# Kernel optimization log

Measured on AMD Instinct MI355X. Metric: run time of the kernel, lower is better.

The kernel has to match this reference:

```python
import jax, jax.numpy as jnp
import numpy as np

N = 100000
E = 1600000
IN_C, HID_C, OUT_C = 40, 64, 3


def _sage_params(key, f_in, f_out):
    k1, k2, k3 = jax.random.split(key, 3)
    s = 1.0 / np.sqrt(f_in)
    return (jax.random.uniform(k1, (f_in, f_out), jnp.float32, -s, s),  # W_neigh (lin_l)
            jax.random.uniform(k2, (f_in, f_out), jnp.float32, -s, s),  # W_root  (lin_r)
            jax.random.uniform(k3, (f_out,), jnp.float32, -s, s))       # bias


def setup_inputs() -> dict:
    key = jax.random.key(0)
    ks = jax.random.split(key, 8)
    x = jax.random.normal(ks[0], (N, IN_C), jnp.float32)
    edge_index = jax.random.randint(ks[1], (2, E), 0, N, jnp.int64)
    dims = [(IN_C, HID_C), (HID_C, HID_C), (HID_C, OUT_C),   # encoder
            (OUT_C, HID_C), (HID_C, HID_C), (HID_C, IN_C)]   # decoder
    names = ['enc1', 'enc2', 'enc3', 'dec1', 'dec2', 'dec3']
    out = {'x': x, 'edge_index': edge_index}
    for name, (fi, fo), k in zip(names, dims, ks[2:]):
        Wl, Wr, b = _sage_params(k, fi, fo)
        out[name + '_Wl'] = Wl
        out[name + '_Wr'] = Wr
        out[name + '_b'] = b
    return out


def _sage_conv(h, src, dst, inv_deg, Wl, Wr, b):
    # mean-aggregate neighbor features (messages src -> dst), then linear.
    msg_sum = jax.ops.segment_sum(h[src], dst, num_segments=N)  # [N, F_in]
    agg = msg_sum * inv_deg                                      # mean aggregation
    return agg @ Wl + h @ Wr + b


def reference(x, edge_index,
              enc1_Wl, enc1_Wr, enc1_b, enc2_Wl, enc2_Wr, enc2_b,
              enc3_Wl, enc3_Wr, enc3_b, dec1_Wl, dec1_Wr, dec1_b,
              dec2_Wl, dec2_Wr, dec2_b, dec3_Wl, dec3_Wr, dec3_b):
    src, dst = edge_index[0], edge_index[1]
    deg = jax.ops.segment_sum(jnp.ones((E,), jnp.float32), dst, num_segments=N)
    inv_deg = (1.0 / jnp.maximum(deg, 1.0))[:, None]
    # encoder
    h = jax.nn.relu(_sage_conv(x, src, dst, inv_deg, enc1_Wl, enc1_Wr, enc1_b))
    h = jax.nn.relu(_sage_conv(h, src, dst, inv_deg, enc2_Wl, enc2_Wr, enc2_b))
    z = _sage_conv(h, src, dst, inv_deg, enc3_Wl, enc3_Wr, enc3_b)
    # decoder
    h = jax.nn.relu(_sage_conv(z, src, dst, inv_deg, dec1_Wl, dec1_Wr, dec1_b))
    h = jax.nn.relu(_sage_conv(h, src, dst, inv_deg, dec2_Wl, dec2_Wr, dec2_b))
    x_rec = _sage_conv(h, src, dst, inv_deg, dec3_Wl, dec3_Wr, dec3_b)
    return (x_rec, z)
```

## Files before the change

### kernel.cpp

```cpp
#include <hip/hip_runtime.h>
#include <stdint.h>

#define NNODES 100000
#define NEDGES 1600000
#define NB 98
#define WIN 25000
#define NSL 32
#define SLICE 50000

typedef unsigned short ushort_t;
typedef __attribute__((ext_vector_type(8))) short bf16x8;
typedef __attribute__((ext_vector_type(4))) float f32x4;

__device__ __forceinline__ float b2f(ushort_t u) {
  union { float f; uint32_t i; } v; v.i = ((uint32_t)u) << 16; return v.f;
}
__device__ __forceinline__ float blo(uint32_t p) {
  union { float f; uint32_t i; } v; v.i = p << 16; return v.f;
}
__device__ __forceinline__ float bhi(uint32_t p) {
  union { float f; uint32_t i; } v; v.i = p & 0xffff0000u; return v.f;
}
__device__ __forceinline__ ushort_t f2b(float f) {
  union { float f; uint32_t i; } v; v.f = f;
  uint32_t r = (v.i + 0x7fffu + ((v.i >> 16) & 1u)) >> 16;
  return (ushort_t)r;
}
__device__ __forceinline__ uint32_t pack2(float lo, float hi) {
  return (uint32_t)f2b(lo) | ((uint32_t)f2b(hi) << 16);
}
__device__ __forceinline__ int clampn(int i) {
  return i < 0 ? 0 : (i >= NNODES ? NNODES - 1 : i);
}

__global__ void detect_k(const uint32_t* __restrict__ x, const uint32_t* __restrict__ ei,
                         int* __restrict__ flags) {
  if (blockIdx.x == 0 && threadIdx.x == 0) {
    int cf = 0, ci = 0;
    for (int i = 0; i < 256; ++i) {
      uint32_t u = x[i];
      uint32_t e = (u >> 7) & 0xFFu;
      if (e >= 100u && e <= 141u) cf++;
      if (ei[2 * i + 1] == 0u) ci++;
    }
    flags[0] = (cf >= 128) ? 1 : 0;
    flags[1] = (ci >= 128) ? 1 : 0;
  }
}

__global__ void zero_i32(int* __restrict__ p, int n) {
  int i = blockIdx.x * blockDim.x + threadIdx.x;
  if (i < n) p[i] = 0;
}

__global__ __launch_bounds__(256) void histw_k(const uint32_t* __restrict__ ei,
                                               int* __restrict__ degp,
                                               const int* __restrict__ flags) {
  __shared__ int h[WIN];
  int b = blockIdx.x;
  int w = b >> 5, s = b & 31;
  for (int j = threadIdx.x; j < WIN; j += 256) h[j] = 0;
  __syncthreads();
  int i64 = flags[1];
  int base = w * WIN;
  int e0 = s * SLICE, e1 = e0 + SLICE;
  for (int e = e0 + threadIdx.x; e < e1; e += 256) {
    int d = i64 ? (int)ei[2 * (size_t)NEDGES + 2 * (size_t)e] : (int)ei[(size_t)NEDGES + e];
    d = clampn(d);
    int j = d - base;
    if ((unsigned)j < (unsigned)WIN) atomicAdd(&h[j], 1);
  }
  __syncthreads();
  int* dp = degp + (size_t)s * NNODES + base;
  for (int j = threadIdx.x; j < WIN; j += 256) dp[j] = h[j];
}

__global__ void hreduce_k(int* __restrict__ degp, int* __restrict__ deg) {
  int n = blockIdx.x * blockDim.x + threadIdx.x;
  if (n >= NNODES) return;
  int run = 0;
  #pragma unroll
  for (int s = 0; s < NSL; ++s) {
    size_t idx = (size_t)s * NNODES + n;
    int t = degp[idx];
    degp[idx] = run;
    run += t;
  }
  deg[n] = run;
}

__global__ __launch_bounds__(1024) void scan1_k(const int* __restrict__ deg, int* __restrict__ bsum) {
  __shared__ int wsum[16];
  int tid = threadIdx.x;
  int i = blockIdx.x * 1024 + tid;
  int v = (i < NNODES) ? deg[i] : 0;
  #pragma unroll
  for (int d = 32; d >= 1; d >>= 1) v += __shfl_down(v, d);
  if ((tid & 63) == 0) wsum[tid >> 6] = v;
  __syncthreads();
  if (tid == 0) {
    int t = 0;
    #pragma unroll
    for (int w = 0; w < 16; ++w) t += wsum[w];
    bsum[blockIdx.x] = t;
  }
}

__global__ void scan2_k(int* __restrict__ bsum, int* __restrict__ offs) {
  if (blockIdx.x == 0 && threadIdx.x == 0) {
    int run = 0;
    for (int b = 0; b < NB; ++b) { int t = bsum[b]; bsum[b] = run; run += t; }
    offs[NNODES] = run;
  }
}

__global__ __launch_bounds__(1024) void scan3_k(const int* __restrict__ deg, const int* __restrict__ bsum,
                                                int* __restrict__ offs, int* __restrict__ cursor,
                                                float* __restrict__ invd) {
  __shared__ int wsum[16];
  int tid = threadIdx.x;
  int lane = tid & 63, wid = tid >> 6;
  int i = blockIdx.x * 1024 + tid;
  int v = (i < NNODES) ? deg[i] : 0;
  int s = v;
  #pragma unroll
  for (int d = 1; d < 64; d <<= 1) {
    int t = __shfl_up(s, d);
    if (lane >= d) s += t;
  }
  if (lane == 63) wsum[wid] = s;
  __syncthreads();
  int wprefix = 0;
  #pragma unroll
  for (int w = 0; w < 16; ++w)
    if (w < wid) wprefix += wsum[w];
  if (i < NNODES) {
    int excl = bsum[blockIdx.x] + wprefix + s - v;
    offs[i] = excl;
    cursor[i] = excl;
    invd[i] = 1.0f / fmaxf((float)v, 1.0f);
  }
}

__global__ __launch_bounds__(256) void scatters_k(const uint32_t* __restrict__ ei,
                                                  const int* __restrict__ offs,
                                                  const int* __restrict__ degp,
                                                  int* __restrict__ csr,
                                                  const int* __restrict__ flags) {
  __shared__ int cur[WIN];
  int b = blockIdx.x;
  int w = b >> 5, s = b & 31;
  int base = w * WIN;
  const int* dp = degp + (size_t)s * NNODES + base;
  for (int j = threadIdx.x; j < WIN; j += 256) cur[j] = offs[base + j] + dp[j];
  __syncthreads();
  int i64 = flags[1];
  int e0 = s * SLICE, e1 = e0 + SLICE;
  for (int e = e0 + threadIdx.x; e < e1; e += 256) {
    int d = i64 ? (int)ei[2 * (size_t)NEDGES + 2 * (size_t)e] : (int)ei[(size_t)NEDGES + e];
    d = clampn(d);
    int j = d - base;
    if ((unsigned)j < (unsigned)WIN) {
      int src = i64 ? (int)ei[2 * (size_t)e] : (int)ei[e];
      int p = atomicAdd(&cur[j], 1);
      if (p >= 0 && p < NEDGES) csr[p] = clampn(src);
    }
  }
}

template <bool BF16>
__global__ void cvt_packx_k(const void* __restrict__ src, uint32_t* __restrict__ dst, int npairs,
                            const int* __restrict__ flags) {
  if (flags[0] != (BF16 ? 1 : 0)) return;
  int i = blockIdx.x * blockDim.x + threadIdx.x;
  if (i < npairs) {
    if constexpr (BF16) dst[i] = ((const uint32_t*)src)[i];
    else {
      const float* s = (const float*)src;
      dst[i] = pack2(s[2 * i], s[2 * i + 1]);
    }
  }
}

template <bool BF16>
__global__ void cvt_outp_k(const uint32_t* __restrict__ src, void* __restrict__ dst, int npairs,
                           const int* __restrict__ flags) {
  if (flags[0] != (BF16 ? 1 : 0)) return;
  int i = blockIdx.x * blockDim.x + threadIdx.x;
  if (i < npairs) {
    if constexpr (BF16) ((uint32_t*)dst)[i] = src[i];
    else {
      uint32_t w = src[i];
      float* d = (float*)dst;
      d[2 * i] = blo(w);
      d[2 * i + 1] = bhi(w);
    }
  }
}

template <bool BF16>
__global__ void cvt_out_k(const float* __restrict__ src, void* __restrict__ dst, int n,
                          const int* __restrict__ flags) {
  if (flags[0] != (BF16 ? 1 : 0)) return;
  int i = blockIdx.x * blockDim.x + threadIdx.x;
  if (i < n) {
    if constexpr (BF16) ((ushort_t*)dst)[i] = f2b(src[i]);
    else ((float*)dst)[i] = src[i];
  }
}

struct WPtrs { const void* p[18]; int sz[18]; int off[18]; };

template <bool BF16>
__global__ void cvt_w_k(WPtrs w, float* __restrict__ dst, const int* __restrict__ flags) {
  if (flags[0] != (BF16 ? 1 : 0)) return;
  int a = blockIdx.x;
  int sz = w.sz[a], off = w.off[a];
  for (int t = threadIdx.x; t < sz; t += blockDim.x) {
    dst[off + t] = BF16 ? b2f(((const ushort_t*)w.p[a])[t]) : ((const float*)w.p[a])[t];
  }
}

template <bool ADD_U>
__global__ __launch_bounds__(256) void agg3_k(const float* __restrict__ feat, const int* __restrict__ csr,
                                              const int* __restrict__ offs, const float* __restrict__ invd,
                                              const float* __restrict__ u, float* __restrict__ out) {
  int n = blockIdx.x * blockDim.x + threadIdx.x;
  if (n >= NNODES) return;
  int k0 = offs[n], k1 = offs[n + 1];
  float a0 = 0.f, a1 = 0.f, a2 = 0.f;
  int k = k0;
  for (; k + 4 <= k1; k += 4) {
    const float* r0 = feat + (size_t)clampn(csr[k]) * 3;
    const float* r1 = feat + (size_t)clampn(csr[k + 1]) * 3;
    const float* r2 = feat + (size_t)clampn(csr[k + 2]) * 3;
    const float* r3 = feat + (size_t)clampn(csr[k + 3]) * 3;
    a0 += r0[0] + r1[0] + r2[0] + r3[0];
    a1 += r0[1] + r1[1] + r2[1] + r3[1];
    a2 += r0[2] + r1[2] + r2[2] + r3[2];
  }
  for (; k < k1; ++k) {
    const float* r = feat + (size_t)clampn(csr[k]) * 3;
    a0 += r[0]; a1 += r[1]; a2 += r[2];
  }
  float iv = invd[n];
  a0 *= iv; a1 *= iv; a2 *= iv;
  if constexpr (ADD_U) {
    a0 += u[(size_t)n * 3];
    a1 += u[(size_t)n * 3 + 1];
    a2 += u[(size_t)n * 3 + 2];
  }
  out[(size_t)n * 3]     = a0;
  out[(size_t)n * 3 + 1] = a1;
  out[(size_t)n * 3 + 2] = a2;
}

template <int PAIRS, bool ADD_U>
__global__ __launch_bounds__(256) void aggp2_k(const uint32_t* __restrict__ feat, const int* __restrict__ csr,
                                               const int* __restrict__ offs, const float* __restrict__ invd,
                                               const uint32_t* __restrict__ u, uint32_t* __restrict__ out) {
  int lane = threadIdx.x & 63;
  int n = (blockIdx.x * blockDim.x + threadIdx.x) >> 6;
  if (n >= NNODES) return;
  int half = lane >> 5;
  int p = lane & 31;
  int k0 = offs[n], k1 = offs[n + 1];
  float aL = 0.f, aH = 0.f;
  int k = k0;
  for (; k + 8 <= k1; k += 8) {
    int i0 = clampn(csr[k + half]), i1 = clampn(csr[k + 2 + half]);
    int i2 = clampn(csr[k + 4 + half]), i3 = clampn(csr[k + 6 + half]);
    if (p < PAIRS) {
      uint32_t w0 = feat[(size_t)i0 * PAIRS + p];
      uint32_t w1 = feat[(size_t)i1 * PAIRS + p];
      uint32_t w2 = feat[(size_t)i2 * PAIRS + p];
      uint32_t w3 = feat[(size_t)i3 * PAIRS + p];
      aL += blo(w0) + blo(w1) + blo(w2) + blo(w3);
      aH += bhi(w0) + bhi(w1) + bhi(w2) + bhi(w3);
    }
  }
  for (; k < k1; k += 2) {
    int kk = k + half;
    if (kk < k1 && p < PAIRS) {
      uint32_t w = feat[(size_t)clampn(csr[kk]) * PAIRS + p];
      aL += blo(w);
      aH += bhi(w);
    }
  }
  aL += __shfl_xor(aL, 32);
  aH += __shfl_xor(aH, 32);
  if (half == 0 && p < PAIRS) {
    float iv = invd[n];
    float vL = aL * iv, vH = aH * iv;
    if constexpr (ADD_U) {
      uint32_t uw = u[(size_t)n * PAIRS + p];
      vL += blo(uw);
      vH += bhi(uw);
    }
    out[(size_t)n * PAIRS + p] = pack2(vL, vH);
  }
}

template <int F_IN, int F_OUT, bool DUAL, bool RELU, bool PIN, bool POUT>
__global__ __launch_bounds__(256) void mgemm_k(const void* __restrict__ Av, const void* __restrict__ Bv,
                                               const float* __restrict__ W1, const float* __restrict__ W2,
                                               const float* __restrict__ Wb,
                                               void* __restrict__ C1v, void* __restrict__ C2v) {
  constexpr int KS = (F_IN + 31) / 32;
  constexpr int JT = (F_OUT + 15) / 16;
  constexpr int PP = F_IN / 2;
  int lane = threadIdx.x & 63;
  int wid  = threadIdx.x >> 6;
  int tile = blockIdx.x * 4 + wid;
  if (tile * 16 >= NNODES) return;
  int l15 = lane & 15, l4 = lane >> 4;

  bf16x8 w1f[KS][JT], w2f[KS][JT];
  float bv[JT];
  #pragma unroll
  for (int ks = 0; ks < KS; ++ks) {
    #pragma unroll
    for (int jt = 0; jt < JT; ++jt) {
      int col = jt * 16 + l15;
      #pragma unroll
      for (int j = 0; j < 8; ++j) {
        int k = ks * 32 + l4 * 8 + j;
        bool ok = (k < F_IN) && (col < F_OUT);
        w1f[ks][jt][j] = ok ? (short)f2b(W1[k * F_OUT + col]) : (short)0;
        w2f[ks][jt][j] = ok ? (short)f2b(W2[k * F_OUT + col]) : (short)0;
      }
    }
  }
  #pragma unroll
  for (int jt = 0; jt < JT; ++jt) {
    int col = jt * 16 + l15;
    bv[jt] = (col < F_OUT) ? Wb[col] : 0.f;
  }

  int row = tile * 16 + l15;
  bf16x8 af[KS], bfr[KS];
  if constexpr (PIN) {
    const uint32_t* Arow = (const uint32_t*)Av + (size_t)row * PP;
    #pragma unroll
    for (int ks = 0; ks < KS; ++ks) {
      #pragma unroll
      for (int w4 = 0; w4 < 4; ++w4) {
        int word = ks * 16 + l4 * 4 + w4;
        uint32_t v = (word < PP) ? Arow[word] : 0u;
        af[ks][2 * w4]     = (short)(v & 0xffffu);
        af[ks][2 * w4 + 1] = (short)(v >> 16);
      }
    }
    if constexpr (!DUAL) {
      const uint32_t* Brow = (const uint32_t*)Bv + (size_t)row * PP;
      #pragma unroll
      for (int ks = 0; ks < KS; ++ks) {
        #pragma unroll
        for (int w4 = 0; w4 < 4; ++w4) {
          int word = ks * 16 + l4 * 4 + w4;
          uint32_t v = (word < PP) ? Brow[word] : 0u;
          bfr[ks][2 * w4]     = (short)(v & 0xffffu);
          bfr[ks][2 * w4 + 1] = (short)(v >> 16);
        }
      }
    }
  } else {
    const float* Arow = (const float*)Av + (size_t)row * F_IN;
    #pragma unroll
    for (int ks = 0; ks < KS; ++ks) {
      #pragma unroll
      for (int j = 0; j < 8; ++j) {
        int k = ks * 32 + l4 * 8 + j;
        af[ks][j] = (k < F_IN) ? (short)f2b(Arow[k]) : (short)0;
      }
    }
    if constexpr (!DUAL) {
      const float* Brow = (const float*)Bv + (size_t)row * F_IN;
      #pragma unroll
      for (int ks = 0; ks < KS; ++ks) {
        #pragma unroll
        for (int j = 0; j < 8; ++j) {
          int k = ks * 32 + l4 * 8 + j;
          bfr[ks][j] = (k < F_IN) ? (short)f2b(Brow[k]) : (short)0;
        }
      }
    }
  }

  f32x4 acc1[JT], acc2[DUAL ? JT : 1];
  #pragma unroll
  for (int jt = 0; jt < JT; ++jt) {
    acc1[jt] = (f32x4)(0.f);
    if constexpr (DUAL) acc2[jt] = (f32x4)(0.f);
  }

  #pragma unroll
  for (int ks = 0; ks < KS; ++ks) {
    #pragma unroll
    for (int jt = 0; jt < JT; ++jt) {
      acc1[jt] = __builtin_amdgcn_mfma_f32_16x16x32_bf16(af[ks], w1f[ks][jt], acc1[jt], 0, 0, 0);
      if constexpr (DUAL)
        acc2[jt] = __builtin_amdgcn_mfma_f32_16x16x32_bf16(af[ks], w2f[ks][jt], acc2[jt], 0, 0, 0);
      else
        acc1[jt] = __builtin_amdgcn_mfma_f32_16x16x32_bf16(bfr[ks], w2f[ks][jt], acc1[jt], 0, 0, 0);
    }
  }

  #pragma unroll
  for (int jt = 0; jt < JT; ++jt) {
    int col = jt * 16 + l15;
    #pragma unroll
    for (int r = 0; r < 4; ++r) {
      int orow = tile * 16 + l4 * 4 + r;
      if constexpr (DUAL) {
        float v1 = acc1[jt][r];
        float v2 = acc2[jt][r] + bv[jt];
        if constexpr (POUT) {
          float p1 = __shfl_xor(v1, 1);
          float p2 = __shfl_xor(v2, 1);
          if (((lane & 1) == 0) && col < F_OUT) {
            ((uint32_t*)C1v)[(size_t)orow * (F_OUT / 2) + (col >> 1)] = pack2(v1, p1);
            ((uint32_t*)C2v)[(size_t)orow * (F_OUT / 2) + (col >> 1)] = pack2(v2, p2);
          }
        } else {
          if (col < F_OUT) {
            ((float*)C1v)[(size_t)orow * F_OUT + col] = v1;
            ((float*)C2v)[(size_t)orow * F_OUT + col] = v2;
          }
        }
      } else {
        float v = acc1[jt][r] + bv[jt];
        if constexpr (RELU) v = fmaxf(v, 0.f);
        if constexpr (POUT) {
          float pv = __shfl_xor(v, 1);
          if (((lane & 1) == 0) && col < F_OUT)
            ((uint32_t*)C1v)[(size_t)orow * (F_OUT / 2) + (col >> 1)] = pack2(v, pv);
        } else {
          if (col < F_OUT)
            ((float*)C1v)[(size_t)orow * F_OUT + col] = v;
        }
      }
    }
  }
}

extern "C" void kernel_launch(void* const* d_in, const int* in_sizes, int n_in,
                              void* d_out, int out_size, void* d_ws, size_t ws_size,
                              hipStream_t stream) {
  const uint32_t* xw = (const uint32_t*)d_in[0];
  const uint32_t* ei = (const uint32_t*)d_in[1];

  char* ws = (char*)d_ws;
  size_t off = 0;
  auto carve = [&](size_t bytes) -> char* {
    char* p = ws + off;
    off = (off + bytes + 255) & ~(size_t)255;
    return p;
  };
  int* flags     = (int*)carve(8);
  int* deg       = (int*)carve((size_t)NNODES * 4);
  int* offs      = (int*)carve((size_t)(NNODES + 1) * 4);
  int* cursor    = (int*)carve((size_t)NNODES * 4);
  float* invd    = (float*)carve((size_t)NNODES * 4);
  int* bsum      = (int*)carve((size_t)NB * 4);
  int* csr       = (int*)carve((size_t)NEDGES * 4);
  float* wf      = (float*)carve((size_t)32768 * 4);
  uint32_t* xp   = (uint32_t*)carve((size_t)NNODES * 20 * 4);
  uint32_t* mp   = (uint32_t*)carve((size_t)NNODES * 20 * 4);
  uint32_t* b0p  = (uint32_t*)carve((size_t)NNODES * 32 * 4);
  uint32_t* b1p  = (uint32_t*)carve((size_t)NNODES * 32 * 4);
  uint32_t* b2p  = (uint32_t*)carve((size_t)NNODES * 32 * 4);
  uint32_t* y40p = (uint32_t*)carve((size_t)NNODES * 20 * 4);
  uint32_t* u40p = (uint32_t*)carve((size_t)NNODES * 20 * 4);
  uint32_t* xrp  = (uint32_t*)carve((size_t)NNODES * 20 * 4);
  float* y3f     = (float*)carve((size_t)NNODES * 3 * 4);
  float* u3f     = (float*)carve((size_t)NNODES * 3 * 4);
  float* zf      = (float*)carve((size_t)NNODES * 3 * 4);
  float* m3f     = (float*)carve((size_t)NNODES * 3 * 4);

  int* degp = (int*)b0p;

  static const int wsz[18] = {2560, 2560, 64, 4096, 4096, 64, 192, 192, 3,
                              192, 192, 64, 4096, 4096, 64, 2560, 2560, 40};
  WPtrs wp;
  int woff = 0;
  for (int i = 0; i < 18; ++i) {
    wp.p[i] = d_in[2 + i];
    wp.sz[i] = wsz[i];
    wp.off[i] = woff;
    woff += wsz[i];
  }
  const float* W[18];
  for (int i = 0; i < 18; ++i) W[i] = wf + wp.off[i];

  detect_k<<<1, 64, 0, stream>>>(xw, ei, flags);
  zero_i32<<<(NEDGES + 255) / 256, 256, 0, stream>>>(csr, NEDGES);
  histw_k<<<128, 256, 0, stream>>>(ei, degp, flags);
  hreduce_k<<<(NNODES + 255) / 256, 256, 0, stream>>>(degp, deg);
  scan1_k<<<NB, 1024, 0, stream>>>(deg, bsum);
  scan2_k<<<1, 64, 0, stream>>>(bsum, offs);
  scan3_k<<<NB, 1024, 0, stream>>>(deg, bsum, offs, cursor, invd);
  scatters_k<<<128, 256, 0, stream>>>(ei, offs, degp, csr, flags);

  const int NXP = NNODES * 20;
  cvt_packx_k<false><<<(NXP + 255) / 256, 256, 0, stream>>>(d_in[0], xp, NXP, flags);
  cvt_packx_k<true ><<<(NXP + 255) / 256, 256, 0, stream>>>(d_in[0], xp, NXP, flags);
  cvt_w_k<false><<<18, 256, 0, stream>>>(wp, wf, flags);
  cvt_w_k<true ><<<18, 256, 0, stream>>>(wp, wf, flags);

  const int AGGW_BLOCKS = (NNODES * 64 + 255) / 256;
  const int AGG3_BLOCKS = (NNODES + 255) / 256;
  const int MG = (NNODES / 16 + 3) / 4;

  aggp2_k<20, false><<<AGGW_BLOCKS, 256, 0, stream>>>(xp, csr, offs, invd, nullptr, mp);
  mgemm_k<40, 64, false, true, true, true><<<MG, 256, 0, stream>>>(mp, xp, W[0], W[1], W[2], b1p, nullptr);
  aggp2_k<32, false><<<AGGW_BLOCKS, 256, 0, stream>>>(b1p, csr, offs, invd, nullptr, b0p);
  mgemm_k<64, 64, false, true, true, true><<<MG, 256, 0, stream>>>(b0p, b1p, W[3], W[4], W[5], b2p, nullptr);
  mgemm_k<64, 3, true, false, true, false><<<MG, 256, 0, stream>>>(b2p, nullptr, W[6], W[7], W[8], y3f, u3f);
  agg3_k<true><<<AGG3_BLOCKS, 256, 0, stream>>>(y3f, csr, offs, invd, u3f, zf);
  agg3_k<false><<<AGG3_BLOCKS, 256, 0, stream>>>(zf, csr, offs, invd, nullptr, m3f);
  mgemm_k<3, 64, false, true, false, true><<<MG, 256, 0, stream>>>(m3f, zf, W[9], W[10], W[11], b1p, nullptr);
  aggp2_k<32, false><<<AGGW_BLOCKS, 256, 0, stream>>>(b1p, csr, offs, invd, nullptr, b0p);
  mgemm_k<64, 64, false, true, true, true><<<MG, 256, 0, stream>>>(b0p, b1p, W[12], W[13], W[14], b2p, nullptr);
  mgemm_k<64, 40, true, false, true, true><<<MG, 256, 0, stream>>>(b2p, nullptr, W[15], W[16], W[17], y40p, u40p);
  aggp2_k<20, true><<<AGGW_BLOCKS, 256, 0, stream>>>(y40p, csr, offs, invd, u40p, xrp);

  const int NX = NNODES * 40;
  const int NZ = NNODES * 3;
  cvt_outp_k<false><<<(NXP + 255) / 256, 256, 0, stream>>>(xrp, d_out, NXP, flags);
  cvt_outp_k<true ><<<(NXP + 255) / 256, 256, 0, stream>>>(xrp, d_out, NXP, flags);
  cvt_out_k<false><<<(NZ + 255) / 256, 256, 0, stream>>>(zf, (float*)d_out + NX, NZ, flags);
  cvt_out_k<true ><<<(NZ + 255) / 256, 256, 0, stream>>>(zf, (ushort_t*)d_out + NX, NZ, flags);
  (void)in_sizes; (void)n_in; (void)out_size; (void)ws_size;
}
```

Before: 595.0 us.

## Replace LDS-windowed CSR scatter with four range-filtered global-atomic scatter passes

The old CSR build ran 128 blocks, each keeping a 25000-entry cursor window in shared memory and scanning one edge slice with LDS atomics. It is replaced by four full-grid passes, each handling one quarter of the destination range and using global atomics on the cursor array. The aim is more parallelism than 128 blocks offer, with the range split keeping atomic traffic localized. In exchange the edge list is read four times and the atomics move from LDS to global memory.

```diff
diff --git a/kernel.cpp b/kernel.cpp
--- a/kernel.cpp
+++ b/kernel.cpp
@@ -142,30 +142,26 @@
   }
 }
 
-__global__ __launch_bounds__(256) void scatters_k(const uint32_t* __restrict__ ei,
-                                                  const int* __restrict__ offs,
-                                                  const int* __restrict__ degp,
-                                                  int* __restrict__ csr,
-                                                  const int* __restrict__ flags) {
-  __shared__ int cur[WIN];
-  int b = blockIdx.x;
-  int w = b >> 5, s = b & 31;
-  int base = w * WIN;
-  const int* dp = degp + (size_t)s * NNODES + base;
-  for (int j = threadIdx.x; j < WIN; j += 256) cur[j] = offs[base + j] + dp[j];
-  __syncthreads();
+__global__ void scatter4_k(const uint32_t* __restrict__ ei, int* __restrict__ cursor,
+                           int* __restrict__ csr, const int* __restrict__ flags,
+                           int lo, int hi) {
+  int e = blockIdx.x * blockDim.x + threadIdx.x;
+  if (e >= NEDGES) return;
   int i64 = flags[1];
-  int e0 = s * SLICE, e1 = e0 + SLICE;
-  for (int e = e0 + threadIdx.x; e < e1; e += 256) {
-    int d = i64 ? (int)ei[2 * (size_t)NEDGES + 2 * (size_t)e] : (int)ei[(size_t)NEDGES + e];
+  int s, d;
+  if (i64) {
+    d = (int)ei[2 * (size_t)NEDGES + 2 * (size_t)e];
     d = clampn(d);
-    int j = d - base;
-    if ((unsigned)j < (unsigned)WIN) {
-      int src = i64 ? (int)ei[2 * (size_t)e] : (int)ei[e];
-      int p = atomicAdd(&cur[j], 1);
-      if (p >= 0 && p < NEDGES) csr[p] = clampn(src);
-    }
-  }
+    if (d < lo || d >= hi) return;
+    s = (int)ei[2 * (size_t)e];
+  } else {
+    d = (int)ei[(size_t)NEDGES + e];
+    d = clampn(d);
+    if (d < lo || d >= hi) return;
+    s = (int)ei[e];
+  }
+  int p = atomicAdd(&cursor[d], 1);
+  if (p >= 0 && p < NEDGES) csr[p] = clampn(s);
 }
 
 template <bool BF16>
@@ -500,7 +496,11 @@
   scan1_k<<<NB, 1024, 0, stream>>>(deg, bsum);
   scan2_k<<<1, 64, 0, stream>>>(bsum, offs);
   scan3_k<<<NB, 1024, 0, stream>>>(deg, bsum, offs, cursor, invd);
-  scatters_k<<<128, 256, 0, stream>>>(ei, offs, degp, csr, flags);
+  const int EB = (NEDGES + 255) / 256;
+  scatter4_k<<<EB, 256, 0, stream>>>(ei, cursor, csr, flags, 0, 25000);
+  scatter4_k<<<EB, 256, 0, stream>>>(ei, cursor, csr, flags, 25000, 50000);
+  scatter4_k<<<EB, 256, 0, stream>>>(ei, cursor, csr, flags, 50000, 75000);
+  scatter4_k<<<EB, 256, 0, stream>>>(ei, cursor, csr, flags, 75000, 100000);
 
   const int NXP = NNODES * 20;
   cvt_packx_k<false><<<(NXP + 255) / 256, 256, 0, stream>>>(d_in[0], xp, NXP, flags);
```

After: 568.8 us. -4.4%, faster.
